# Optimization experiments

Measured on AMD Instinct MI355X. Metric: run time of the kernel, lower is better.

Reference implementation:

```python
import jax, jax.numpy as jnp
import numpy as np

BATCH, SEQ_LEN, N_FEATURES = 4096, 128, 32
# (input_size, hidden_size) for encoder_l1..l3, decoder_l1..l3
SIZES = [(N_FEATURES, 16), (16, 4), (4, 1), (1, 4), (4, 8), (8, 16)]
NAMES = ["e1", "e2", "e3", "d1", "d2", "d3"]


def setup_inputs() -> dict:
    key = jax.random.key(0)
    keys = jax.random.split(key, 27)
    inp = {"x": jax.random.normal(keys[0], (BATCH, SEQ_LEN, N_FEATURES), jnp.float32)}
    ki = 1
    for name, (din, h) in zip(NAMES, SIZES):
        s = 1.0 / np.sqrt(h)
        inp[name + "_Wih"] = jax.random.uniform(keys[ki], (4 * h, din), jnp.float32, -s, s); ki += 1
        inp[name + "_Whh"] = jax.random.uniform(keys[ki], (4 * h, h), jnp.float32, -s, s); ki += 1
        inp[name + "_bih"] = jax.random.uniform(keys[ki], (4 * h,), jnp.float32, -s, s); ki += 1
        inp[name + "_bhh"] = jax.random.uniform(keys[ki], (4 * h,), jnp.float32, -s, s); ki += 1
    s = 1.0 / np.sqrt(16)
    inp["Wout"] = jax.random.uniform(keys[25], (N_FEATURES, 16), jnp.float32, -s, s)
    inp["bout"] = jax.random.uniform(keys[26], (N_FEATURES,), jnp.float32, -s, s)
    return inp


def lstm(x, Wih, Whh, bih, bhh):
    """Single-layer batch_first LSTM, PyTorch gate order (i, f, g, o).
    x: [B, S, Din] -> [B, S, H] (h0 = c0 = 0)."""
    B = x.shape[0]
    H = Whh.shape[1]
    b = bih + bhh
    # Precompute input projections for all timesteps at once: [S, B, 4H]
    xg = jnp.einsum("bsd,gd->sbg", x, Wih) + b

    def step(carry, xg_t):
        h, c = carry
        gates = xg_t + h @ Whh.T  # [B, 4H]
        i, f, g, o = jnp.split(gates, 4, axis=-1)
        i = jax.nn.sigmoid(i)
        f = jax.nn.sigmoid(f)
        g = jnp.tanh(g)
        o = jax.nn.sigmoid(o)
        c = f * c + i * g
        h = o * jnp.tanh(c)
        return (h, c), h

    h0 = jnp.zeros((B, H), x.dtype)
    (_, _), hs = jax.lax.scan(step, (h0, h0), xg)
    return jnp.swapaxes(hs, 0, 1)  # [B, S, H]


def reference(x,
              e1_Wih, e1_Whh, e1_bih, e1_bhh,
              e2_Wih, e2_Whh, e2_bih, e2_bhh,
              e3_Wih, e3_Whh, e3_bih, e3_bhh,
              d1_Wih, d1_Whh, d1_bih, d1_bhh,
              d2_Wih, d2_Whh, d2_bih, d2_bhh,
              d3_Wih, d3_Whh, d3_bih, d3_bhh,
              Wout, bout):
    # Dropout layers are identity in eval mode.
    h = lstm(x, e1_Wih, e1_Whh, e1_bih, e1_bhh)
    h = lstm(h, e2_Wih, e2_Whh, e2_bih, e2_bhh)
    h = lstm(h, e3_Wih, e3_Whh, e3_bih, e3_bhh)
    enc = h[:, -1, :]                                   # [B, 1]
    h = jnp.broadcast_to(enc[:, None, :], (x.shape[0], SEQ_LEN, enc.shape[-1]))
    h = lstm(h, d1_Wih, d1_Whh, d1_bih, d1_bhh)
    h = lstm(h, d2_Wih, d2_Whh, d2_bih, d2_bhh)
    h = lstm(h, d3_Wih, d3_Whh, d3_bih, d3_bhh)
    return h @ Wout.T + bout                            # [B, S, n_features]
```

## Files before the change

### kernel.cpp

```cpp
#include <hip/hip_runtime.h>

#define LOG2E 1.44269504088896340736f

__device__ __forceinline__ float vexp2(float x){ float r; asm("v_exp_f32 %0, %1" : "=v"(r) : "v"(x)); return r; }
__device__ __forceinline__ float vrcp (float x){ float r; asm("v_rcp_f32 %0, %1" : "=v"(r) : "v"(x)); return r; }
template<int OFF> __device__ __forceinline__ float dsw(float v){
  return __int_as_float(__builtin_amdgcn_ds_swizzle(__float_as_int(v), OFF));
}
#define SWX(m)  dsw<((m)<<10)|0x1F>
#define BC16(k) dsw<((k)<<5)|0x10>
__device__ __forceinline__ float sigm(float x){ return vrcp(1.0f + vexp2(x * (-LOG2E))); }
__device__ __forceinline__ float tanh_f(float x){
  float s = vrcp(1.0f + vexp2(x * (-2.0f*LOG2E)));
  return s + s - 1.0f;
}

__global__ void __launch_bounds__(256)
lstm_ae_fused(const float* __restrict__ x,
              const float* __restrict__ e1Wi, const float* __restrict__ e1Wh, const float* __restrict__ e1bi, const float* __restrict__ e1bh,
              const float* __restrict__ e2Wi, const float* __restrict__ e2Wh, const float* __restrict__ e2bi, const float* __restrict__ e2bh,
              const float* __restrict__ e3Wi, const float* __restrict__ e3Wh, const float* __restrict__ e3bi, const float* __restrict__ e3bh,
              const float* __restrict__ d1Wi, const float* __restrict__ d1Wh, const float* __restrict__ d1bi, const float* __restrict__ d1bh,
              const float* __restrict__ d2Wi, const float* __restrict__ d2Wh, const float* __restrict__ d2bi, const float* __restrict__ d2bh,
              const float* __restrict__ d3Wi, const float* __restrict__ d3Wh, const float* __restrict__ d3bi, const float* __restrict__ d3bh,
              const float* __restrict__ Wout, const float* __restrict__ bout,
              float* __restrict__ out)
{
  const int tid  = threadIdx.x;
  const int lane = tid & 63;
  const int wv   = tid >> 6;
  const int gw   = blockIdx.x*4 + wv;
  const int bA   = gw*2, bB = gw*2 + 1;
  const float* __restrict__ xbA = x + (size_t)bA * 4096;
  const float* __restrict__ xbB = x + (size_t)bB * 4096;
  float* __restrict__ obA = out + (size_t)bA * 4096;
  float* __restrict__ obB = out + (size_t)bB * 4096;

  __shared__ float s_e1[13*64*4];
  __shared__ float s_e2[16*20];
  __shared__ float s_eb2[16];
  __shared__ float s_e3[4*8];
  __shared__ float s_d1[16*8];
  __shared__ float s_d2[32*20];
  __shared__ float s_d3[7*64*4];
  __shared__ float s_wo[32*20];
  __shared__ float s_x [4][512];
  __shared__ float s_h1[4][64];
  __shared__ float s_g1[4][64];
  __shared__ float s_g2[4][64];
  __shared__ float s_g3[4][64];

  if (tid < 64){
    const int l = tid;
    const float A1l = (l>=32 && l<48) ? 2.f : 1.f;
    for (int k=0;k<32;++k) s_e1[((k>>2)*64+l)*4+(k&3)]      = e1Wi[l*32+k]*A1l;
    for (int k=0;k<16;++k) s_e1[(((k>>2)+8)*64+l)*4+(k&3)]  = e1Wh[l*16+k]*A1l;
    s_e1[(12*64+l)*4] = (e1bi[l]+e1bh[l])*A1l;
    for (int k=0;k<8;++k)  s_d3[((k>>2)*64+l)*4+(k&3)]      = d3Wi[l*8+k]*A1l;
    for (int k=0;k<16;++k) s_d3[(((k>>2)+2)*64+l)*4+(k&3)]  = d3Wh[l*16+k]*A1l;
    s_d3[(6*64+l)*4] = (d3bi[l]+d3bh[l])*A1l;
    if (l < 16){
      const float A2l = (l>=8 && l<12) ? 2.f : 1.f;
      for (int k=0;k<16;++k) s_e2[l*20+k]    = e2Wi[l*16+k]*A2l;
      for (int k=0;k<4;++k)  s_e2[l*20+16+k] = e2Wh[l*4+k]*A2l;
      s_eb2[l] = (e2bi[l]+e2bh[l])*A2l;
      for (int k=0;k<4;++k)  s_d1[l*8+k] = d1Wh[l*4+k]*A2l;
      s_d1[l*8+4] = d1Wi[l]*A2l;
      s_d1[l*8+5] = (d1bi[l]+d1bh[l])*A2l;
    }
    if (l < 4){
      const float A3l = (l==2) ? 2.f : 1.f;
      for (int k=0;k<4;++k) s_e3[l*8+k] = e3Wi[l*4+k]*A3l;
      s_e3[l*8+4] = e3Wh[l]*A3l;
      s_e3[l*8+5] = (e3bi[l]+e3bh[l])*A3l;
    }
    if (l < 32){
      const float AD2l = (l>=16 && l<24) ? 2.f : 1.f;
      for (int k=0;k<4;++k) s_d2[l*20+k]   = d2Wi[l*4+k]*AD2l;
      for (int k=0;k<8;++k) s_d2[l*20+4+k] = d2Wh[l*8+k]*AD2l;
      s_d2[l*20+12] = (d2bi[l]+d2bh[l])*AD2l;
      for (int k=0;k<16;++k) s_wo[l*20+k] = Wout[l*16+k];
      s_wo[l*20+16] = bout[l];
    }
  }
  __syncthreads();

  const bool isg1 = (lane >= 32) && (lane < 48);
  const bool isg2 = ((lane & 15) >= 8) && ((lane & 15) < 12);
  const bool isg3 = ((lane & 3) == 2);
  const bool isgD2= ((lane & 31) >= 16) && ((lane & 31) < 24);
  const float A1 = isg1 ? 2.f : 1.f,  B1 = isg1 ? -1.f : 0.f;
  const float A2 = isg2 ? 2.f : 1.f,  B2 = isg2 ? -1.f : 0.f;
  const float A3 = isg3 ? 2.f : 1.f,  B3 = isg3 ? -1.f : 0.f;
  const float AD2= isgD2? 2.f : 1.f,  BD2= isgD2? -1.f : 0.f;
  const bool selA = ((lane & 16) == 0);
  const int  h16  = lane & 16;
  const int  h32  = lane & 32;
  const int  h32s = (lane & 32) >> 1;

  const float4* e1v = (const float4*)s_e1;
  const float4* d3v = (const float4*)s_d3;
  const float* r2  = &s_e2[(lane&15)*20];
  const float* r3  = &s_e3[(lane&3)*8];
  const float* rd1 = &s_d1[(lane&15)*8];
  const float* rd2 = &s_d2[(lane&31)*20];
  const float* rw  = &s_wo[(lane&31)*20];

  float h3b = 0.f;

  {
    float4 w1q[8], wh1q[4];
    #pragma unroll
    for (int g=0; g<8; ++g) w1q[g] = e1v[g*64+lane];
    #pragma unroll
    for (int g=0; g<4; ++g) wh1q[g] = e1v[(8+g)*64+lane];
    const float eb1 = s_e1[(12*64+lane)*4];
    float4 w2q0 = *(const float4*)(r2);
    float4 w2q1 = *(const float4*)(r2+4);
    float4 w2q2 = *(const float4*)(r2+8);
    float4 w2q3 = *(const float4*)(r2+12);
    float4 w2q4 = *(const float4*)(r2+16);
    const float eb2 = s_eb2[lane&15];
    float4 w30 = *(const float4*)(r3);
    const float w3h = r3[4], eb3 = r3[5];

    s_h1[wv][lane] = 0.f;
    float c1 = 0.f, c2 = 0.f, c3 = 0.f;
    float bc2_0 = 0.f, bc2_1 = 0.f, bc2_2 = 0.f, bc2_3 = 0.f;

    float4 pfA = ((const float4*)xbA)[lane];
    float4 pfB = ((const float4*)xbB)[lane];

    for (int tc=0; tc<128; tc+=8){
      ((float4*)&s_x[wv][0])[lane]   = pfA;
      ((float4*)&s_x[wv][256])[lane] = pfB;
      if (tc + 8 < 128){
        pfA = ((const float4*)(xbA + (tc+8)*32))[lane];
        pfB = ((const float4*)(xbB + (tc+8)*32))[lane];
      }
      float xga[8], xgb[8];
      #pragma unroll
      for (int tt=0; tt<8; ++tt){
        const float4* xA4 = (const float4*)&s_x[wv][tt*32];
        const float4* xB4 = (const float4*)&s_x[wv][256+tt*32];
        float pa0=eb1, pa1=0.f, pa2=0.f, pa3=0.f;
        float pb0=eb1, pb1=0.f, pb2=0.f, pb3=0.f;
        #pragma unroll
        for (int g=0; g<8; ++g){
          float4 w = w1q[g];
          float4 xa = xA4[g], xb = xB4[g];
          pa0 = fmaf(w.x, xa.x, pa0);  pb0 = fmaf(w.x, xb.x, pb0);
          pa1 = fmaf(w.y, xa.y, pa1);  pb1 = fmaf(w.y, xb.y, pb1);
          pa2 = fmaf(w.z, xa.z, pa2);  pb2 = fmaf(w.z, xb.z, pb2);
          pa3 = fmaf(w.w, xa.w, pa3);  pb3 = fmaf(w.w, xb.w, pb3);
        }
        xga[tt] = (pa0+pa1)+(pa2+pa3);
        xgb[tt] = (pb0+pb1)+(pb2+pb3);
      }
      #pragma unroll
      for (int tt=0; tt<8; ++tt){
        const float4* h1A = (const float4*)&s_h1[wv][0];
        const float4* h1B = (const float4*)&s_h1[wv][16];
        float aA0 = xga[tt], aA1=0.f, aA2=0.f, aA3=0.f;
        float aB0 = xgb[tt], aB1=0.f, aB2=0.f, aB3=0.f;
        #pragma unroll
        for (int g=0; g<4; ++g){
          float4 w = wh1q[g];
          float4 ha = h1A[g], hb = h1B[g];
          aA0 = fmaf(w.x, ha.x, aA0);  aB0 = fmaf(w.x, hb.x, aB0);
          aA1 = fmaf(w.y, ha.y, aA1);  aB1 = fmaf(w.y, hb.y, aB1);
          aA2 = fmaf(w.z, ha.z, aA2);  aB2 = fmaf(w.z, hb.z, aB2);
          aA3 = fmaf(w.w, ha.w, aA3);  aB3 = fmaf(w.w, hb.w, aB3);
        }
        float vA = fmaf(sigm((aA0+aA1)+(aA2+aA3)), A1, B1);
        float vB = fmaf(sigm((aB0+aB1)+(aB2+aB3)), A1, B1);
        float t1A = SWX(16)(vA);
        float t2A = __shfl_xor(vA, 32, 64);
        float t3A = SWX(16)(t2A);
        float t1B = SWX(16)(vB);
        float t2B = __shfl_xor(vB, 32, 64);
        float t3B = SWX(16)(t2B);
        float ip = selA ? vA  : t1B;
        float fp = selA ? t1A : vB;
        float gp = selA ? t2A : t3B;
        float op = selA ? t3A : t2B;
        c1 = fmaf(fp, c1, ip*gp);
        float h1v = op * tanh_f(c1);
        s_h1[wv][lane] = h1v;

        const float4* h1s = (const float4*)&s_h1[wv][h16];
        float4 q0 = h1s[0], q1 = h1s[1], q2 = h1s[2], q3 = h1s[3];
        float a0 = eb2, a1 = 0.f;
        a0 = fmaf(w2q0.x,q0.x,a0);  a1 = fmaf(w2q0.y,q0.y,a1);
        a0 = fmaf(w2q0.z,q0.z,a0);  a1 = fmaf(w2q0.w,q0.w,a1);
        a0 = fmaf(w2q1.x,q1.x,a0);  a1 = fmaf(w2q1.y,q1.y,a1);
        a0 = fmaf(w2q1.z,q1.z,a0);  a1 = fmaf(w2q1.w,q1.w,a1);
        a0 = fmaf(w2q2.x,q2.x,a0);  a1 = fmaf(w2q2.y,q2.y,a1);
        a0 = fmaf(w2q2.z,q2.z,a0);  a1 = fmaf(w2q2.w,q2.w,a1);
        a0 = fmaf(w2q3.x,q3.x,a0);  a1 = fmaf(w2q3.y,q3.y,a1);
        a0 = fmaf(w2q3.z,q3.z,a0);  a1 = fmaf(w2q3.w,q3.w,a1);
        a0 = fmaf(w2q4.x,bc2_0,a0); a1 = fmaf(w2q4.y,bc2_1,a1);
        a0 = fmaf(w2q4.z,bc2_2,a0); a1 = fmaf(w2q4.w,bc2_3,a1);
        float v2 = fmaf(sigm(a0+a1), A2, B2);
        float f2 = SWX(4)(v2), g2 = SWX(8)(v2), o2 = SWX(12)(v2);
        c2 = fmaf(f2, c2, v2*g2);
        float h2v = o2 * tanh_f(c2);
        bc2_0 = BC16(0)(h2v); bc2_1 = BC16(1)(h2v);
        bc2_2 = BC16(2)(h2v); bc2_3 = BC16(3)(h2v);

        float a = fmaf(w3h, h3b, eb3);
        a = fmaf(w30.x, bc2_0, a);
        a = fmaf(w30.y, bc2_1, a);
        a = fmaf(w30.z, bc2_2, a);
        a = fmaf(w30.w, bc2_3, a);
        float v3 = fmaf(sigm(a), A3, B3);
        float f3 = SWX(1)(v3), g3 = SWX(2)(v3), o3 = SWX(3)(v3);
        c3 = fmaf(f3, c3, v3*g3);
        h3b = BC16(0)(o3 * tanh_f(c3));
      }
    }
  }

  {
    const float encv = h3b;
    const float p1  = fmaf(rd1[4], encv, rd1[5]);
    const float bd2 = rd2[12];
    const float bd3 = s_d3[(6*64+lane)*4];
    const float bo  = rw[16];
    float4 wd1 = *(const float4*)(rd1);
    float4 w2a = *(const float4*)(rd2);
    float4 w2b = *(const float4*)(rd2+4);
    float4 w2c = *(const float4*)(rd2+8);
    float4 d3q[6];
    #pragma unroll
    for (int g=0; g<6; ++g) d3q[g] = d3v[g*64+lane];
    float4 woa = *(const float4*)(rw);
    float4 wob = *(const float4*)(rw+4);
    float4 woc = *(const float4*)(rw+8);
    float4 wod = *(const float4*)(rw+12);

    s_g1[wv][lane] = 0.f;  s_g2[wv][lane] = 0.f;  s_g3[wv][lane] = 0.f;
    float dc1 = 0.f, dc2 = 0.f, dc3 = 0.f;
    float* __restrict__ obSel = (lane < 32) ? (obA + lane) : (obB + lane - 32);

    for (int t=0; t<128; ++t){
      float4 g1q = *(const float4*)&s_g1[wv][h16];
      float a0 = p1, a1 = 0.f;
      a0 = fmaf(wd1.x, g1q.x, a0); a1 = fmaf(wd1.y, g1q.y, a1);
      a0 = fmaf(wd1.z, g1q.z, a0); a1 = fmaf(wd1.w, g1q.w, a1);
      float v1 = fmaf(sigm(a0+a1), A2, B2);
      float f1 = SWX(4)(v1), gg1 = SWX(8)(v1), o1 = SWX(12)(v1);
      dc1 = fmaf(f1, dc1, v1*gg1);
      float h1v = o1 * tanh_f(dc1);
      s_g1[wv][lane] = h1v;

      float4 g1s = *(const float4*)&s_g1[wv][h32s];
      float4 g2a = *(const float4*)&s_g2[wv][h32];
      float4 g2b = *(const float4*)&s_g2[wv][h32+4];
      a0 = bd2; a1 = 0.f;
      a0 = fmaf(w2a.x, g1s.x, a0); a1 = fmaf(w2a.y, g1s.y, a1);
      a0 = fmaf(w2a.z, g1s.z, a0); a1 = fmaf(w2a.w, g1s.w, a1);
      a0 = fmaf(w2b.x, g2a.x, a0); a1 = fmaf(w2b.y, g2a.y, a1);
      a0 = fmaf(w2b.z, g2a.z, a0); a1 = fmaf(w2b.w, g2a.w, a1);
      a0 = fmaf(w2c.x, g2b.x, a0); a1 = fmaf(w2c.y, g2b.y, a1);
      a0 = fmaf(w2c.z, g2b.z, a0); a1 = fmaf(w2c.w, g2b.w, a1);
      float v2 = fmaf(sigm(a0+a1), AD2, BD2);
      float f2 = SWX(8)(v2), gg2 = SWX(16)(v2), o2 = SWX(24)(v2);
      dc2 = fmaf(f2, dc2, v2*gg2);
      float h2v = o2 * tanh_f(dc2);
      s_g2[wv][lane] = h2v;

      const float4* g2A = (const float4*)&s_g2[wv][0];
      const float4* g2B = (const float4*)&s_g2[wv][32];
      const float4* g3A = (const float4*)&s_g3[wv][0];
      const float4* g3B = (const float4*)&s_g3[wv][16];
      float aA0=bd3, aA1=0.f, aA2=0.f, aA3=0.f;
      float aB0=bd3, aB1=0.f, aB2=0.f, aB3=0.f;
      #pragma unroll
      for (int grp=0; grp<2; ++grp){
        float4 wq = d3q[grp];
        float4 ha = g2A[grp], hb = g2B[grp];
        aA0 = fmaf(wq.x, ha.x, aA0);  aB0 = fmaf(wq.x, hb.x, aB0);
        aA1 = fmaf(wq.y, ha.y, aA1);  aB1 = fmaf(wq.y, hb.y, aB1);
        aA2 = fmaf(wq.z, ha.z, aA2);  aB2 = fmaf(wq.z, hb.z, aB2);
        aA3 = fmaf(wq.w, ha.w, aA3);  aB3 = fmaf(wq.w, hb.w, aB3);
      }
      #pragma unroll
      for (int grp=0; grp<4; ++grp){
        float4 wq = d3q[2+grp];
        float4 ha = g3A[grp], hb = g3B[grp];
        aA0 = fmaf(wq.x, ha.x, aA0);  aB0 = fmaf(wq.x, hb.x, aB0);
        aA1 = fmaf(wq.y, ha.y, aA1);  aB1 = fmaf(wq.y, hb.y, aB1);
        aA2 = fmaf(wq.z, ha.z, aA2);  aB2 = fmaf(wq.z, hb.z, aB2);
        aA3 = fmaf(wq.w, ha.w, aA3);  aB3 = fmaf(wq.w, hb.w, aB3);
      }
      float vA = fmaf(sigm((aA0+aA1)+(aA2+aA3)), A1, B1);
      float vB = fmaf(sigm((aB0+aB1)+(aB2+aB3)), A1, B1);
      float t1A = SWX(16)(vA);
      float t2A = __shfl_xor(vA, 32, 64);
      float t3A = SWX(16)(t2A);
      float t1B = SWX(16)(vB);
      float t2B = __shfl_xor(vB, 32, 64);
      float t3B = SWX(16)(t2B);
      float ip = selA ? vA  : t1B;
      float fp = selA ? t1A : vB;
      float gp = selA ? t2A : t3B;
      float op = selA ? t3A : t2B;
      dc3 = fmaf(fp, dc3, ip*gp);
      float h3v = op * tanh_f(dc3);
      s_g3[wv][lane] = h3v;

      const float4* g3s = (const float4*)&s_g3[wv][h32s];
      float4 u0 = g3s[0], u1 = g3s[1], u2 = g3s[2], u3 = g3s[3];
      float ov0 = bo, ov1 = 0.f;
      ov0 = fmaf(woa.x, u0.x, ov0);  ov1 = fmaf(woa.y, u0.y, ov1);
      ov0 = fmaf(woa.z, u0.z, ov0);  ov1 = fmaf(woa.w, u0.w, ov1);
      ov0 = fmaf(wob.x, u1.x, ov0);  ov1 = fmaf(wob.y, u1.y, ov1);
      ov0 = fmaf(wob.z, u1.z, ov0);  ov1 = fmaf(wob.w, u1.w, ov1);
      ov0 = fmaf(woc.x, u2.x, ov0);  ov1 = fmaf(woc.y, u2.y, ov1);
      ov0 = fmaf(woc.z, u2.z, ov0);  ov1 = fmaf(woc.w, u2.w, ov1);
      ov0 = fmaf(wod.x, u3.x, ov0);  ov1 = fmaf(wod.y, u3.y, ov1);
      ov0 = fmaf(wod.z, u3.z, ov0);  ov1 = fmaf(wod.w, u3.w, ov1);
      obSel[t*32] = ov0 + ov1;
    }
  }
}

extern "C" void kernel_launch(void* const* d_in, const int* in_sizes, int n_in,
                              void* d_out, int out_size, void* d_ws, size_t ws_size,
                              hipStream_t stream) {
  (void)in_sizes; (void)n_in; (void)d_ws; (void)ws_size; (void)out_size;
  const float* x    = (const float*)d_in[0];
  const float* e1Wi = (const float*)d_in[1];
  const float* e1Wh = (const float*)d_in[2];
  const float* e1bi = (const float*)d_in[3];
  const float* e1bh = (const float*)d_in[4];
  const float* e2Wi = (const float*)d_in[5];
  const float* e2Wh = (const float*)d_in[6];
  const float* e2bi = (const float*)d_in[7];
  const float* e2bh = (const float*)d_in[8];
  const float* e3Wi = (const float*)d_in[9];
  const float* e3Wh = (const float*)d_in[10];
  const float* e3bi = (const float*)d_in[11];
  const float* e3bh = (const float*)d_in[12];
  const float* d1Wi = (const float*)d_in[13];
  const float* d1Wh = (const float*)d_in[14];
  const float* d1bi = (const float*)d_in[15];
  const float* d1bh = (const float*)d_in[16];
  const float* d2Wi = (const float*)d_in[17];
  const float* d2Wh = (const float*)d_in[18];
  const float* d2bi = (const float*)d_in[19];
  const float* d2bh = (const float*)d_in[20];
  const float* d3Wi = (const float*)d_in[21];
  const float* d3Wh = (const float*)d_in[22];
  const float* d3bi = (const float*)d_in[23];
  const float* d3bh = (const float*)d_in[24];
  const float* Wout = (const float*)d_in[25];
  const float* boutp= (const float*)d_in[26];
  float* out = (float*)d_out;

  lstm_ae_fused<<<512, 256, 0, stream>>>(x,
      e1Wi, e1Wh, e1bi, e1bh,
      e2Wi, e2Wh, e2bi, e2bh,
      e3Wi, e3Wh, e3bi, e3bh,
      d1Wi, d1Wh, d1bi, d1bh,
      d2Wi, d2Wh, d2bi, d2bh,
      d3Wi, d3Wh, d3bi, d3bh,
      Wout, boutp, out);
}
```

Before: 221.8 us.

## Wavefront-skew stacked LSTM layers so each timestep's layers run independently

Restructures the encoder and decoder recurrences as a diagonal (wavefront) pipeline. In each iteration, layer k works on timestep t-k, so the per-layer computations no longer depend on each other within an iteration. All LDS reads are issued up front and all state writes are deferred to the end of the iteration. The aim is more instruction-level parallelism, hiding the long serial chain of sigmoid, tanh and swizzle latency between layers. The cost is prologue and epilogue code, more live registers, and larger code size from unrolling.

```diff
diff --git a/kernel.cpp b/kernel.cpp
--- a/kernel.cpp
+++ b/kernel.cpp
@@ -130,15 +130,15 @@
 
     float4 pfA = ((const float4*)xbA)[lane];
     float4 pfB = ((const float4*)xbB)[lane];
-
-    for (int tc=0; tc<128; tc+=8){
+    float xga[8], xgb[8];
+
+    auto stage_and_xg = [&](int tc){
       ((float4*)&s_x[wv][0])[lane]   = pfA;
       ((float4*)&s_x[wv][256])[lane] = pfB;
       if (tc + 8 < 128){
         pfA = ((const float4*)(xbA + (tc+8)*32))[lane];
         pfB = ((const float4*)(xbB + (tc+8)*32))[lane];
       }
-      float xga[8], xgb[8];
       #pragma unroll
       for (int tt=0; tt<8; ++tt){
         const float4* xA4 = (const float4*)&s_x[wv][tt*32];
@@ -157,21 +157,40 @@
         xga[tt] = (pa0+pa1)+(pa2+pa3);
         xgb[tt] = (pb0+pb1)+(pb2+pb3);
       }
-      #pragma unroll
-      for (int tt=0; tt<8; ++tt){
+    };
+
+    auto enc_iter = [&](int D1_, int D2_, int D3_, float xa, float xb){
+      float4 ha0,ha1,ha2,ha3,hb0,hb1,hb2,hb3,qq0,qq1,qq2,qq3;
+      float h1new = 0.f, nb0=0.f, nb1=0.f, nb2=0.f, nb3=0.f;
+      if (D1_){
         const float4* h1A = (const float4*)&s_h1[wv][0];
         const float4* h1B = (const float4*)&s_h1[wv][16];
-        float aA0 = xga[tt], aA1=0.f, aA2=0.f, aA3=0.f;
-        float aB0 = xgb[tt], aB1=0.f, aB2=0.f, aB3=0.f;
-        #pragma unroll
-        for (int g=0; g<4; ++g){
-          float4 w = wh1q[g];
-          float4 ha = h1A[g], hb = h1B[g];
-          aA0 = fmaf(w.x, ha.x, aA0);  aB0 = fmaf(w.x, hb.x, aB0);
-          aA1 = fmaf(w.y, ha.y, aA1);  aB1 = fmaf(w.y, hb.y, aB1);
-          aA2 = fmaf(w.z, ha.z, aA2);  aB2 = fmaf(w.z, hb.z, aB2);
-          aA3 = fmaf(w.w, ha.w, aA3);  aB3 = fmaf(w.w, hb.w, aB3);
-        }
+        ha0=h1A[0]; ha1=h1A[1]; ha2=h1A[2]; ha3=h1A[3];
+        hb0=h1B[0]; hb1=h1B[1]; hb2=h1B[2]; hb3=h1B[3];
+      }
+      if (D2_){
+        const float4* h1s = (const float4*)&s_h1[wv][h16];
+        qq0=h1s[0]; qq1=h1s[1]; qq2=h1s[2]; qq3=h1s[3];
+      }
+      if (D1_){
+        float aA0 = xa, aA1=0.f, aA2=0.f, aA3=0.f;
+        float aB0 = xb, aB1=0.f, aB2=0.f, aB3=0.f;
+        aA0=fmaf(wh1q[0].x,ha0.x,aA0); aB0=fmaf(wh1q[0].x,hb0.x,aB0);
+        aA1=fmaf(wh1q[0].y,ha0.y,aA1); aB1=fmaf(wh1q[0].y,hb0.y,aB1);
+        aA2=fmaf(wh1q[0].z,ha0.z,aA2); aB2=fmaf(wh1q[0].z,hb0.z,aB2);
+        aA3=fmaf(wh1q[0].w,ha0.w,aA3); aB3=fmaf(wh1q[0].w,hb0.w,aB3);
+        aA0=fmaf(wh1q[1].x,ha1.x,aA0); aB0=fmaf(wh1q[1].x,hb1.x,aB0);
+        aA1=fmaf(wh1q[1].y,ha1.y,aA1); aB1=fmaf(wh1q[1].y,hb1.y,aB1);
+        aA2=fmaf(wh1q[1].z,ha1.z,aA2); aB2=fmaf(wh1q[1].z,hb1.z,aB2);
+        aA3=fmaf(wh1q[1].w,ha1.w,aA3); aB3=fmaf(wh1q[1].w,hb1.w,aB3);
+        aA0=fmaf(wh1q[2].x,ha2.x,aA0); aB0=fmaf(wh1q[2].x,hb2.x,aB0);
+        aA1=fmaf(wh1q[2].y,ha2.y,aA1); aB1=fmaf(wh1q[2].y,hb2.y,aB1);
+        aA2=fmaf(wh1q[2].z,ha2.z,aA2); aB2=fmaf(wh1q[2].z,hb2.z,aB2);
+        aA3=fmaf(wh1q[2].w,ha2.w,aA3); aB3=fmaf(wh1q[2].w,hb2.w,aB3);
+        aA0=fmaf(wh1q[3].x,ha3.x,aA0); aB0=fmaf(wh1q[3].x,hb3.x,aB0);
+        aA1=fmaf(wh1q[3].y,ha3.y,aA1); aB1=fmaf(wh1q[3].y,hb3.y,aB1);
+        aA2=fmaf(wh1q[3].z,ha3.z,aA2); aB2=fmaf(wh1q[3].z,hb3.z,aB2);
+        aA3=fmaf(wh1q[3].w,ha3.w,aA3); aB3=fmaf(wh1q[3].w,hb3.w,aB3);
         float vA = fmaf(sigm((aA0+aA1)+(aA2+aA3)), A1, B1);
         float vB = fmaf(sigm((aB0+aB1)+(aB2+aB3)), A1, B1);
         float t1A = SWX(16)(vA);
@@ -185,29 +204,28 @@
         float gp = selA ? t2A : t3B;
         float op = selA ? t3A : t2B;
         c1 = fmaf(fp, c1, ip*gp);
-        float h1v = op * tanh_f(c1);
-        s_h1[wv][lane] = h1v;
-
-        const float4* h1s = (const float4*)&s_h1[wv][h16];
-        float4 q0 = h1s[0], q1 = h1s[1], q2 = h1s[2], q3 = h1s[3];
+        h1new = op * tanh_f(c1);
+      }
+      if (D2_){
         float a0 = eb2, a1 = 0.f;
-        a0 = fmaf(w2q0.x,q0.x,a0);  a1 = fmaf(w2q0.y,q0.y,a1);
-        a0 = fmaf(w2q0.z,q0.z,a0);  a1 = fmaf(w2q0.w,q0.w,a1);
-        a0 = fmaf(w2q1.x,q1.x,a0);  a1 = fmaf(w2q1.y,q1.y,a1);
-        a0 = fmaf(w2q1.z,q1.z,a0);  a1 = fmaf(w2q1.w,q1.w,a1);
-        a0 = fmaf(w2q2.x,q2.x,a0);  a1 = fmaf(w2q2.y,q2.y,a1);
-        a0 = fmaf(w2q2.z,q2.z,a0);  a1 = fmaf(w2q2.w,q2.w,a1);
-        a0 = fmaf(w2q3.x,q3.x,a0);  a1 = fmaf(w2q3.y,q3.y,a1);
-        a0 = fmaf(w2q3.z,q3.z,a0);  a1 = fmaf(w2q3.w,q3.w,a1);
-        a0 = fmaf(w2q4.x,bc2_0,a0); a1 = fmaf(w2q4.y,bc2_1,a1);
-        a0 = fmaf(w2q4.z,bc2_2,a0); a1 = fmaf(w2q4.w,bc2_3,a1);
+        a0 = fmaf(w2q0.x,qq0.x,a0);  a1 = fmaf(w2q0.y,qq0.y,a1);
+        a0 = fmaf(w2q0.z,qq0.z,a0);  a1 = fmaf(w2q0.w,qq0.w,a1);
+        a0 = fmaf(w2q1.x,qq1.x,a0);  a1 = fmaf(w2q1.y,qq1.y,a1);
+        a0 = fmaf(w2q1.z,qq1.z,a0);  a1 = fmaf(w2q1.w,qq1.w,a1);
+        a0 = fmaf(w2q2.x,qq2.x,a0);  a1 = fmaf(w2q2.y,qq2.y,a1);
+        a0 = fmaf(w2q2.z,qq2.z,a0);  a1 = fmaf(w2q2.w,qq2.w,a1);
+        a0 = fmaf(w2q3.x,qq3.x,a0);  a1 = fmaf(w2q3.y,qq3.y,a1);
+        a0 = fmaf(w2q3.z,qq3.z,a0);  a1 = fmaf(w2q3.w,qq3.w,a1);
+        a0 = fmaf(w2q4.x,bc2_0,a0);  a1 = fmaf(w2q4.y,bc2_1,a1);
+        a0 = fmaf(w2q4.z,bc2_2,a0);  a1 = fmaf(w2q4.w,bc2_3,a1);
         float v2 = fmaf(sigm(a0+a1), A2, B2);
         float f2 = SWX(4)(v2), g2 = SWX(8)(v2), o2 = SWX(12)(v2);
         c2 = fmaf(f2, c2, v2*g2);
         float h2v = o2 * tanh_f(c2);
-        bc2_0 = BC16(0)(h2v); bc2_1 = BC16(1)(h2v);
-        bc2_2 = BC16(2)(h2v); bc2_3 = BC16(3)(h2v);
-
+        nb0 = BC16(0)(h2v); nb1 = BC16(1)(h2v);
+        nb2 = BC16(2)(h2v); nb3 = BC16(3)(h2v);
+      }
+      if (D3_){
         float a = fmaf(w3h, h3b, eb3);
         a = fmaf(w30.x, bc2_0, a);
         a = fmaf(w30.y, bc2_1, a);
@@ -218,7 +236,22 @@
         c3 = fmaf(f3, c3, v3*g3);
         h3b = BC16(0)(o3 * tanh_f(c3));
       }
+      if (D1_) s_h1[wv][lane] = h1new;
+      if (D2_){ bc2_0 = nb0; bc2_1 = nb1; bc2_2 = nb2; bc2_3 = nb3; }
+    };
+
+    stage_and_xg(0);
+    enc_iter(1,0,0, xga[0], xgb[0]);
+    enc_iter(1,1,0, xga[1], xgb[1]);
+    #pragma unroll
+    for (int tt=2; tt<8; ++tt) enc_iter(1,1,1, xga[tt], xgb[tt]);
+    for (int tc=8; tc<128; tc+=8){
+      stage_and_xg(tc);
+      #pragma unroll
+      for (int tt=0; tt<8; ++tt) enc_iter(1,1,1, xga[tt], xgb[tt]);
     }
+    enc_iter(0,1,1, 0.f, 0.f);
+    enc_iter(0,0,1, 0.f, 0.f);
   }
 
   {
@@ -243,86 +276,119 @@
     float dc1 = 0.f, dc2 = 0.f, dc3 = 0.f;
     float* __restrict__ obSel = (lane < 32) ? (obA + lane) : (obB + lane - 32);
 
-    for (int t=0; t<128; ++t){
-      float4 g1q = *(const float4*)&s_g1[wv][h16];
-      float a0 = p1, a1 = 0.f;
-      a0 = fmaf(wd1.x, g1q.x, a0); a1 = fmaf(wd1.y, g1q.y, a1);
-      a0 = fmaf(wd1.z, g1q.z, a0); a1 = fmaf(wd1.w, g1q.w, a1);
-      float v1 = fmaf(sigm(a0+a1), A2, B2);
-      float f1 = SWX(4)(v1), gg1 = SWX(8)(v1), o1 = SWX(12)(v1);
-      dc1 = fmaf(f1, dc1, v1*gg1);
-      float h1v = o1 * tanh_f(dc1);
-      s_g1[wv][lane] = h1v;
-
-      float4 g1s = *(const float4*)&s_g1[wv][h32s];
-      float4 g2a = *(const float4*)&s_g2[wv][h32];
-      float4 g2b = *(const float4*)&s_g2[wv][h32+4];
-      a0 = bd2; a1 = 0.f;
-      a0 = fmaf(w2a.x, g1s.x, a0); a1 = fmaf(w2a.y, g1s.y, a1);
-      a0 = fmaf(w2a.z, g1s.z, a0); a1 = fmaf(w2a.w, g1s.w, a1);
-      a0 = fmaf(w2b.x, g2a.x, a0); a1 = fmaf(w2b.y, g2a.y, a1);
-      a0 = fmaf(w2b.z, g2a.z, a0); a1 = fmaf(w2b.w, g2a.w, a1);
-      a0 = fmaf(w2c.x, g2b.x, a0); a1 = fmaf(w2c.y, g2b.y, a1);
-      a0 = fmaf(w2c.z, g2b.z, a0); a1 = fmaf(w2c.w, g2b.w, a1);
-      float v2 = fmaf(sigm(a0+a1), AD2, BD2);
-      float f2 = SWX(8)(v2), gg2 = SWX(16)(v2), o2 = SWX(24)(v2);
-      dc2 = fmaf(f2, dc2, v2*gg2);
-      float h2v = o2 * tanh_f(dc2);
-      s_g2[wv][lane] = h2v;
-
-      const float4* g2A = (const float4*)&s_g2[wv][0];
-      const float4* g2B = (const float4*)&s_g2[wv][32];
-      const float4* g3A = (const float4*)&s_g3[wv][0];
-      const float4* g3B = (const float4*)&s_g3[wv][16];
-      float aA0=bd3, aA1=0.f, aA2=0.f, aA3=0.f;
-      float aB0=bd3, aB1=0.f, aB2=0.f, aB3=0.f;
-      #pragma unroll
-      for (int grp=0; grp<2; ++grp){
-        float4 wq = d3q[grp];
-        float4 ha = g2A[grp], hb = g2B[grp];
-        aA0 = fmaf(wq.x, ha.x, aA0);  aB0 = fmaf(wq.x, hb.x, aB0);
-        aA1 = fmaf(wq.y, ha.y, aA1);  aB1 = fmaf(wq.y, hb.y, aB1);
-        aA2 = fmaf(wq.z, ha.z, aA2);  aB2 = fmaf(wq.z, hb.z, aB2);
-        aA3 = fmaf(wq.w, ha.w, aA3);  aB3 = fmaf(wq.w, hb.w, aB3);
-      }
-      #pragma unroll
-      for (int grp=0; grp<4; ++grp){
-        float4 wq = d3q[2+grp];
-        float4 ha = g3A[grp], hb = g3B[grp];
-        aA0 = fmaf(wq.x, ha.x, aA0);  aB0 = fmaf(wq.x, hb.x, aB0);
-        aA1 = fmaf(wq.y, ha.y, aA1);  aB1 = fmaf(wq.y, hb.y, aB1);
-        aA2 = fmaf(wq.z, ha.z, aA2);  aB2 = fmaf(wq.z, hb.z, aB2);
-        aA3 = fmaf(wq.w, ha.w, aA3);  aB3 = fmaf(wq.w, hb.w, aB3);
-      }
-      float vA = fmaf(sigm((aA0+aA1)+(aA2+aA3)), A1, B1);
-      float vB = fmaf(sigm((aB0+aB1)+(aB2+aB3)), A1, B1);
-      float t1A = SWX(16)(vA);
-      float t2A = __shfl_xor(vA, 32, 64);
-      float t3A = SWX(16)(t2A);
-      float t1B = SWX(16)(vB);
-      float t2B = __shfl_xor(vB, 32, 64);
-      float t3B = SWX(16)(t2B);
-      float ip = selA ? vA  : t1B;
-      float fp = selA ? t1A : vB;
-      float gp = selA ? t2A : t3B;
-      float op = selA ? t3A : t2B;
-      dc3 = fmaf(fp, dc3, ip*gp);
-      float h3v = op * tanh_f(dc3);
-      s_g3[wv][lane] = h3v;
-
-      const float4* g3s = (const float4*)&s_g3[wv][h32s];
-      float4 u0 = g3s[0], u1 = g3s[1], u2 = g3s[2], u3 = g3s[3];
-      float ov0 = bo, ov1 = 0.f;
-      ov0 = fmaf(woa.x, u0.x, ov0);  ov1 = fmaf(woa.y, u0.y, ov1);
-      ov0 = fmaf(woa.z, u0.z, ov0);  ov1 = fmaf(woa.w, u0.w, ov1);
-      ov0 = fmaf(wob.x, u1.x, ov0);  ov1 = fmaf(wob.y, u1.y, ov1);
-      ov0 = fmaf(wob.z, u1.z, ov0);  ov1 = fmaf(wob.w, u1.w, ov1);
-      ov0 = fmaf(woc.x, u2.x, ov0);  ov1 = fmaf(woc.y, u2.y, ov1);
-      ov0 = fmaf(woc.z, u2.z, ov0);  ov1 = fmaf(woc.w, u2.w, ov1);
-      ov0 = fmaf(wod.x, u3.x, ov0);  ov1 = fmaf(wod.y, u3.y, ov1);
-      ov0 = fmaf(wod.z, u3.z, ov0);  ov1 = fmaf(wod.w, u3.w, ov1);
-      obSel[t*32] = ov0 + ov1;
-    }
+    auto dec_iter = [&](int D1_, int D2_, int D3_, int DL_, int TO){
+      float4 g1q, g1s, g2a, g2b, p2a0, p2a1, p2b0, p2b1;
+      float4 r3a0,r3a1,r3a2,r3a3, r3b0,r3b1,r3b2,r3b3, u0,u1,u2,u3;
+      float g1new=0.f, g2new=0.f, g3new=0.f, ovv=0.f;
+      if (D1_) g1q = *(const float4*)&s_g1[wv][h16];
+      if (D2_){
+        g1s = *(const float4*)&s_g1[wv][h32s];
+        g2a = *(const float4*)&s_g2[wv][h32];
+        g2b = *(const float4*)&s_g2[wv][h32+4];
+      }
+      if (D3_){
+        const float4* g2A = (const float4*)&s_g2[wv][0];
+        const float4* g2B = (const float4*)&s_g2[wv][32];
+        p2a0=g2A[0]; p2a1=g2A[1]; p2b0=g2B[0]; p2b1=g2B[1];
+        const float4* g3A = (const float4*)&s_g3[wv][0];
+        const float4* g3B = (const float4*)&s_g3[wv][16];
+        r3a0=g3A[0]; r3a1=g3A[1]; r3a2=g3A[2]; r3a3=g3A[3];
+        r3b0=g3B[0]; r3b1=g3B[1]; r3b2=g3B[2]; r3b3=g3B[3];
+      }
+      if (DL_){
+        const float4* g3s = (const float4*)&s_g3[wv][h32s];
+        u0=g3s[0]; u1=g3s[1]; u2=g3s[2]; u3=g3s[3];
+      }
+      if (D1_){
+        float a0 = p1, a1 = 0.f;
+        a0 = fmaf(wd1.x, g1q.x, a0); a1 = fmaf(wd1.y, g1q.y, a1);
+        a0 = fmaf(wd1.z, g1q.z, a0); a1 = fmaf(wd1.w, g1q.w, a1);
+        float v1 = fmaf(sigm(a0+a1), A2, B2);
+        float f1 = SWX(4)(v1), gg1 = SWX(8)(v1), o1 = SWX(12)(v1);
+        dc1 = fmaf(f1, dc1, v1*gg1);
+        g1new = o1 * tanh_f(dc1);
+      }
+      if (D2_){
+        float a0 = bd2, a1 = 0.f;
+        a0 = fmaf(w2a.x, g1s.x, a0); a1 = fmaf(w2a.y, g1s.y, a1);
+        a0 = fmaf(w2a.z, g1s.z, a0); a1 = fmaf(w2a.w, g1s.w, a1);
+        a0 = fmaf(w2b.x, g2a.x, a0); a1 = fmaf(w2b.y, g2a.y, a1);
+        a0 = fmaf(w2b.z, g2a.z, a0); a1 = fmaf(w2b.w, g2a.w, a1);
+        a0 = fmaf(w2c.x, g2b.x, a0); a1 = fmaf(w2c.y, g2b.y, a1);
+        a0 = fmaf(w2c.z, g2b.z, a0); a1 = fmaf(w2c.w, g2b.w, a1);
+        float v2 = fmaf(sigm(a0+a1), AD2, BD2);
+        float f2 = SWX(8)(v2), gg2 = SWX(16)(v2), o2 = SWX(24)(v2);
+        dc2 = fmaf(f2, dc2, v2*gg2);
+        g2new = o2 * tanh_f(dc2);
+      }
+      if (D3_){
+        float aA0=bd3, aA1=0.f, aA2=0.f, aA3=0.f;
+        float aB0=bd3, aB1=0.f, aB2=0.f, aB3=0.f;
+        aA0=fmaf(d3q[0].x,p2a0.x,aA0); aB0=fmaf(d3q[0].x,p2b0.x,aB0);
+        aA1=fmaf(d3q[0].y,p2a0.y,aA1); aB1=fmaf(d3q[0].y,p2b0.y,aB1);
+        aA2=fmaf(d3q[0].z,p2a0.z,aA2); aB2=fmaf(d3q[0].z,p2b0.z,aB2);
+        aA3=fmaf(d3q[0].w,p2a0.w,aA3); aB3=fmaf(d3q[0].w,p2b0.w,aB3);
+        aA0=fmaf(d3q[1].x,p2a1.x,aA0); aB0=fmaf(d3q[1].x,p2b1.x,aB0);
+        aA1=fmaf(d3q[1].y,p2a1.y,aA1); aB1=fmaf(d3q[1].y,p2b1.y,aB1);
+        aA2=fmaf(d3q[1].z,p2a1.z,aA2); aB2=fmaf(d3q[1].z,p2b1.z,aB2);
+        aA3=fmaf(d3q[1].w,p2a1.w,aA3); aB3=fmaf(d3q[1].w,p2b1.w,aB3);
+        aA0=fmaf(d3q[2].x,r3a0.x,aA0); aB0=fmaf(d3q[2].x,r3b0.x,aB0);
+        aA1=fmaf(d3q[2].y,r3a0.y,aA1); aB1=fmaf(d3q[2].y,r3b0.y,aB1);
+        aA2=fmaf(d3q[2].z,r3a0.z,aA2); aB2=fmaf(d3q[2].z,r3b0.z,aB2);
+        aA3=fmaf(d3q[2].w,r3a0.w,aA3); aB3=fmaf(d3q[2].w,r3b0.w,aB3);
+        aA0=fmaf(d3q[3].x,r3a1.x,aA0); aB0=fmaf(d3q[3].x,r3b1.x,aB0);
+        aA1=fmaf(d3q[3].y,r3a1.y,aA1); aB1=fmaf(d3q[3].y,r3b1.y,aB1);
+        aA2=fmaf(d3q[3].z,r3a1.z,aA2); aB2=fmaf(d3q[3].z,r3b1.z,aB2);
+        aA3=fmaf(d3q[3].w,r3a1.w,aA3); aB3=fmaf(d3q[3].w,r3b1.w,aB3);
+        aA0=fmaf(d3q[4].x,r3a2.x,aA0); aB0=fmaf(d3q[4].x,r3b2.x,aB0);
+        aA1=fmaf(d3q[4].y,r3a2.y,aA1); aB1=fmaf(d3q[4].y,r3b2.y,aB1);
+        aA2=fmaf(d3q[4].z,r3a2.z,aA2); aB2=fmaf(d3q[4].z,r3b2.z,aB2);
+        aA3=fmaf(d3q[4].w,r3a2.w,aA3); aB3=fmaf(d3q[4].w,r3b2.w,aB3);
+        aA0=fmaf(d3q[5].x,r3a3.x,aA0); aB0=fmaf(d3q[5].x,r3b3.x,aB0);
+        aA1=fmaf(d3q[5].y,r3a3.y,aA1); aB1=fmaf(d3q[5].y,r3b3.y,aB1);
+        aA2=fmaf(d3q[5].z,r3a3.z,aA2); aB2=fmaf(d3q[5].z,r3b3.z,aB2);
+        aA3=fmaf(d3q[5].w,r3a3.w,aA3); aB3=fmaf(d3q[5].w,r3b3.w,aB3);
+        float vA = fmaf(sigm((aA0+aA1)+(aA2+aA3)), A1, B1);
+        float vB = fmaf(sigm((aB0+aB1)+(aB2+aB3)), A1, B1);
+        float t1A = SWX(16)(vA);
+        float t2A = __shfl_xor(vA, 32, 64);
+        float t3A = SWX(16)(t2A);
+        float t1B = SWX(16)(vB);
+        float t2B = __shfl_xor(vB, 32, 64);
+        float t3B = SWX(16)(t2B);
+        float ip = selA ? vA  : t1B;
+        float fp = selA ? t1A : vB;
+        float gp = selA ? t2A : t3B;
+        float op = selA ? t3A : t2B;
+        dc3 = fmaf(fp, dc3, ip*gp);
+        g3new = op * tanh_f(dc3);
+      }
+      if (DL_){
+        float ov0 = bo, ov1 = 0.f;
+        ov0 = fmaf(woa.x, u0.x, ov0);  ov1 = fmaf(woa.y, u0.y, ov1);
+        ov0 = fmaf(woa.z, u0.z, ov0);  ov1 = fmaf(woa.w, u0.w, ov1);
+        ov0 = fmaf(wob.x, u1.x, ov0);  ov1 = fmaf(wob.y, u1.y, ov1);
+        ov0 = fmaf(wob.z, u1.z, ov0);  ov1 = fmaf(wob.w, u1.w, ov1);
+        ov0 = fmaf(woc.x, u2.x, ov0);  ov1 = fmaf(woc.y, u2.y, ov1);
+        ov0 = fmaf(woc.z, u2.z, ov0);  ov1 = fmaf(woc.w, u2.w, ov1);
+        ov0 = fmaf(wod.x, u3.x, ov0);  ov1 = fmaf(wod.y, u3.y, ov1);
+        ov0 = fmaf(wod.z, u3.z, ov0);  ov1 = fmaf(wod.w, u3.w, ov1);
+        ovv = ov0 + ov1;
+      }
+      if (D1_) s_g1[wv][lane] = g1new;
+      if (D2_) s_g2[wv][lane] = g2new;
+      if (D3_) s_g3[wv][lane] = g3new;
+      if (DL_) obSel[TO*32] = ovv;
+    };
+
+    dec_iter(1,0,0,0, 0);
+    dec_iter(1,1,0,0, 0);
+    dec_iter(1,1,1,0, 0);
+    #pragma unroll 2
+    for (int i=3; i<128; ++i) dec_iter(1,1,1,1, i-3);
+    dec_iter(0,1,1,1, 125);
+    dec_iter(0,0,1,1, 126);
+    dec_iter(0,0,0,1, 127);
   }
 }
 
```

New measurement: 196.7 us. -11.3%, faster.
